# Kernel tuning notes

Measured on AMD Instinct MI355X. Metric: run time of the kernel, lower is better.

Reference implementation:

```python
import jax, jax.numpy as jnp
import numpy as np
import math

B, S, D, H = 2, 2048, 1024, 16
DK = D // H


def setup_inputs() -> dict:
    key = jax.random.key(0)
    ks = jax.random.split(key, 11)
    s = 1.0 / math.sqrt(D)
    return {
        "q": jax.random.normal(ks[0], (B, S, D), jnp.float32),
        "k": jax.random.normal(ks[1], (B, S, D), jnp.float32),
        "v": jax.random.normal(ks[2], (B, S, D), jnp.float32),
        "Wq": jax.random.normal(ks[3], (D, D), jnp.float32) * s,
        "bq": jnp.zeros((D,), jnp.float32),
        "Wk": jax.random.normal(ks[4], (D, D), jnp.float32) * s,
        "bk": jnp.zeros((D,), jnp.float32),
        "Wv": jax.random.normal(ks[5], (D, D), jnp.float32) * s,
        "bv": jnp.zeros((D,), jnp.float32),
        "Wo": jax.random.normal(ks[6], (D, D), jnp.float32) * s,
        "bo": jnp.zeros((D,), jnp.float32),
        "mask": jnp.ones((B, 1, S), dtype=bool),
    }


def reference(q, k, v, Wq, bq, Wk, bk, Wv, bv, Wo, bo, mask):
    # project and split heads: [B,S,D] -> [B,H,S,DK]
    def proj(x, W, b):
        return (x @ W.T + b).reshape(B, S, H, DK).transpose(0, 2, 1, 3)

    qh, kh, vh = proj(q, Wq, bq), proj(k, Wk, bk), proj(v, Wv, bv)
    scores = jnp.einsum("bhqd,bhkd->bhqk", qh, kh) / math.sqrt(DK)
    # 3D mask [B,1,S], self-attn: expand to [B,1,S,S] via outer AND
    m = mask[:, :, None, :] & mask[:, :, :, None]
    scores = jnp.where(m, scores, -1e9)
    attn = jax.nn.softmax(scores, axis=-1)
    attn = jnp.nan_to_num(attn, nan=0.0, posinf=0.0, neginf=0.0)
    out = jnp.einsum("bhqk,bhkd->bhqd", attn, vh)  # [B,H,S,DK]
    concat = out.transpose(0, 2, 1, 3).reshape(B, S, D)
    return concat @ Wo.T + bo
```

## Files before the change

### kernel.cpp

```cpp
#include <hip/hip_runtime.h>
#include <hip/hip_bf16.h>
#include <stdint.h>

using bf16 = __bf16;
typedef __attribute__((ext_vector_type(8))) __bf16 bf16x8;
typedef __attribute__((ext_vector_type(4))) __bf16 bf16x4;
typedef __attribute__((ext_vector_type(2))) __bf16 bf16x2;
typedef __attribute__((ext_vector_type(4))) float f32x4;

typedef const __attribute__((address_space(1))) void* gptr_t;
typedef __attribute__((address_space(3))) void* lptr_t;

__device__ __forceinline__ void gld16(const void* g, void* l) {
    __builtin_amdgcn_global_load_lds((gptr_t)g, (lptr_t)l, 16, 0, 0);
}

__global__ __launch_bounds__(256)
void cvt4_kern(const float* __restrict__ w0, const float* __restrict__ w1,
               const float* __restrict__ w2, const float* __restrict__ w3,
               bf16* __restrict__ o0, bf16* __restrict__ o1,
               bf16* __restrict__ o2, bf16* __restrict__ o3, int n)
{
    const int z = blockIdx.y;
    const float* in = z == 0 ? w0 : z == 1 ? w1 : z == 2 ? w2 : w3;
    bf16* out      = z == 0 ? o0 : z == 1 ? o1 : z == 2 ? o2 : o3;
    const int i = (blockIdx.x * 256 + threadIdx.x) * 8;
    if (i >= n) return;
    const float4 f0 = *(const float4*)(in + i);
    const float4 f1 = *(const float4*)(in + i + 4);
    bf16x8 v = { (bf16)f0.x, (bf16)f0.y, (bf16)f0.z, (bf16)f0.w,
                 (bf16)f1.x, (bf16)f1.y, (bf16)f1.z, (bf16)f1.w };
    *(bf16x8*)(out + i) = v;
}

__global__ __launch_bounds__(256)
void cvt3_kern(const float* __restrict__ x0, const float* __restrict__ x1,
               const float* __restrict__ x2,
               bf16* __restrict__ o0, bf16* __restrict__ o1,
               bf16* __restrict__ o2, int n)
{
    const int z = blockIdx.y;
    const float* in = z == 0 ? x0 : z == 1 ? x1 : x2;
    bf16* out      = z == 0 ? o0 : z == 1 ? o1 : o2;
    const int i = (blockIdx.x * 256 + threadIdx.x) * 8;
    if (i >= n) return;
    const float4 f0 = *(const float4*)(in + i);
    const float4 f1 = *(const float4*)(in + i + 4);
    bf16x8 v = { (bf16)f0.x, (bf16)f0.y, (bf16)f0.z, (bf16)f0.w,
                 (bf16)f1.x, (bf16)f1.y, (bf16)f1.z, (bf16)f1.w };
    *(bf16x8*)(out + i) = v;
}

template<bool XBF16, bool OUTF32>
__global__ __launch_bounds__(256, 3)
void gemm_qkv(const void* __restrict__ X0, const void* __restrict__ X1,
              const void* __restrict__ X2,
              const bf16* __restrict__ W0, const bf16* __restrict__ W1,
              const bf16* __restrict__ W2,
              const float* __restrict__ b0, const float* __restrict__ b1,
              const float* __restrict__ b2,
              void* __restrict__ Y0, void* __restrict__ Y1,
              void* __restrict__ Y2)
{
    constexpr int K = 1024, N = 1024, NT = K / 64;
    __shared__ bf16 smem[17408];
    bf16* As = smem;
    bf16* Bs = smem + 8192;

    const int z = blockIdx.z;
    const void*  Xv   = z == 0 ? X0 : z == 1 ? X1 : X2;
    const bf16*  W    = z == 0 ? W0 : z == 1 ? W1 : W2;
    const float* bias = z == 0 ? b0 : z == 1 ? b1 : b2;
    void*        Yv   = z == 0 ? Y0 : z == 1 ? Y1 : Y2;
    const int mode = (z == 2) ? 1 : 0;

    const int t = threadIdx.x;
    const int w = t >> 6, lane = t & 63, quad = lane >> 4, l15 = lane & 15;
    const int m0 = blockIdx.y * 128, n0 = blockIdx.x * 128;
    const int wm = (w >> 1) * 64, wn = (w & 1) * 64;

    const int srow = t >> 3;
    const int sseg = (t & 7) ^ (srow & 7);

    const float* Xf   = (const float*)Xv;
    const bf16*  gA16 = (const bf16*)Xv + (size_t)(m0 + srow) * K + sseg * 8;
    const bf16*  gB   = W + (size_t)(n0 + srow) * K + sseg * 8;

    f32x4 acc[4][4] = {};

    for (int kk = 0; kk < NT; ++kk) {
        const int k0 = kk * 64;
        if constexpr (XBF16) {
            #pragma unroll
            for (int r = 0; r < 4; ++r)
                gld16(gA16 + k0 + r * 32 * K, As + t * 8 + r * 2048);
        } else {
            #pragma unroll
            for (int r = 0; r < 4; ++r) {
                const int row = r * 32 + (t >> 3), sg = t & 7;
                const float* p = Xf + (size_t)(m0 + row) * K + k0 + sg * 8;
                const float4 f0 = *(const float4*)p;
                const float4 f1 = *(const float4*)(p + 4);
                bf16x8 vv = { (bf16)f0.x, (bf16)f0.y, (bf16)f0.z, (bf16)f0.w,
                              (bf16)f1.x, (bf16)f1.y, (bf16)f1.z, (bf16)f1.w };
                *(bf16x8*)&As[row * 64 + ((sg ^ (row & 7)) * 8)] = vv;
            }
        }
        #pragma unroll
        for (int r = 0; r < 4; ++r)
            gld16(gB + k0 + r * 32 * K, Bs + t * 8 + r * 2048);
        __syncthreads();

        bf16x8 af[4][2], bfr[4][2];
        #pragma unroll
        for (int mt = 0; mt < 4; ++mt)
            #pragma unroll
            for (int kt = 0; kt < 2; ++kt) {
                const int row = wm + mt * 16 + l15;
                const int seg = (kt * 4 + quad) ^ (row & 7);
                af[mt][kt] = *(const bf16x8*)&As[row * 64 + seg * 8];
            }
        #pragma unroll
        for (int nt = 0; nt < 4; ++nt)
            #pragma unroll
            for (int kt = 0; kt < 2; ++kt) {
                const int row = wn + nt * 16 + l15;
                const int seg = (kt * 4 + quad) ^ (row & 7);
                bfr[nt][kt] = *(const bf16x8*)&Bs[row * 64 + seg * 8];
            }
        #pragma unroll
        for (int kt = 0; kt < 2; ++kt)
            #pragma unroll
            for (int mt = 0; mt < 4; ++mt)
                #pragma unroll
                for (int nt = 0; nt < 4; ++nt)
                    acc[mt][nt] = __builtin_amdgcn_mfma_f32_16x16x32_bf16(
                        af[mt][kt], bfr[nt][kt], acc[mt][nt], 0, 0, 0);
        __syncthreads();
    }

    if (OUTF32 || mode == 0) {
        #pragma unroll
        for (int nt = 0; nt < 4; ++nt) {
            const int col = n0 + wn + nt * 16 + l15;
            const float bv = bias[col];
            #pragma unroll
            for (int mt = 0; mt < 4; ++mt)
                #pragma unroll
                for (int i = 0; i < 4; ++i) {
                    const int row = m0 + wm + mt * 16 + quad * 4 + i;
                    const float v = acc[mt][nt][i] + bv;
                    const size_t off = (size_t)row * N + col;
                    if (OUTF32) ((float*)Yv)[off] = v;
                    else        ((bf16*)Yv)[off]  = (bf16)v;
                }
        }
    } else {
        constexpr int LDT = 136;
        bf16* Tt = smem;
        #pragma unroll
        for (int nt = 0; nt < 4; ++nt) {
            const int col = wn + nt * 16 + l15;
            const float bv = bias[n0 + col];
            #pragma unroll
            for (int mt = 0; mt < 4; ++mt) {
                const int row0 = wm + mt * 16 + quad * 4;
                bf16x4 vv = { (bf16)(acc[mt][nt][0] + bv),
                              (bf16)(acc[mt][nt][1] + bv),
                              (bf16)(acc[mt][nt][2] + bv),
                              (bf16)(acc[mt][nt][3] + bv) };
                *(bf16x4*)&Tt[col * LDT + row0] = vv;
            }
        }
        __syncthreads();
        const int col = t >> 1, half = t & 1;
        const int gcol = n0 + col;
        const int h = gcol >> 6, d = gcol & 63;
        const int b = m0 >> 11, sb = (m0 & 2047) + half * 64;
        bf16* outp = (bf16*)Yv + (((size_t)(b * 16 + h) * 64 + d) << 11) + sb;
        #pragma unroll
        for (int j = 0; j < 8; ++j)
            *(bf16x8*)(outp + j * 8) =
                *(const bf16x8*)&Tt[col * LDT + half * 64 + j * 8];
    }
}

__global__ __launch_bounds__(512, 4)
void attn_mfma(const bf16* __restrict__ Q, const bf16* __restrict__ Kg,
               const bf16* __restrict__ Vt, bf16* Cc)
{
    constexpr int S = 2048, D = 1024, DK = 64, LDP = 72;
    constexpr int NTS = S / 64;
    __shared__ bf16 Qs[128 * 64];
    __shared__ bf16 Ks[2][64 * 64];
    __shared__ bf16 Vs[2][64 * 64];
    __shared__ bf16 Ps[8][16 * LDP];

    const int t = threadIdx.x;
    const int w = t >> 6, lane = t & 63, quad = lane >> 4, l15 = lane & 15;
    const int bh = blockIdx.y, b = bh >> 4, h = bh & 15;
    const int q0 = blockIdx.x * 128;
    const int wq = w * 16;

    const int srow = t >> 3;
    const int sseg = (t & 7) ^ (srow & 7);

    const bf16* gQ = Q + (size_t)(b * S + q0 + srow) * D + h * DK + sseg * 8;
    const bf16* gK = Kg + (size_t)(b * S + srow) * D + h * DK + sseg * 8;
    const bf16* gV = Vt + ((size_t)bh * DK + srow) * S + sseg * 8;

    gld16(gQ,                  Qs + t * 8);
    gld16(gQ + (size_t)64 * D, Qs + t * 8 + 4096);
    gld16(gK,                  Ks[0] + t * 8);
    gld16(gV,                  Vs[0] + t * 8);
    gld16(gK + (size_t)64 * D, Ks[1] + t * 8);
    gld16(gV + 64,             Vs[1] + t * 8);
    __syncthreads();

    bf16x8 aq[2];
    #pragma unroll
    for (int kt = 0; kt < 2; ++kt) {
        const int row = wq + l15;
        const int seg = (kt * 4 + quad) ^ (row & 7);
        aq[kt] = *(const bf16x8*)&Qs[row * 64 + seg * 8];
    }

    const bf16 onev = (l15 == 0) ? (bf16)1.0f : (bf16)0.0f;
    const bf16x8 bden = { onev, onev, onev, onev, onev, onev, onev, onev };

    f32x4 o[5] = {};
    float m = -1e30f;

    const float c = 0.125f * 1.44269504088896340736f;

    for (int ts = 0; ts < NTS; ++ts) {
        const int cur = ts & 1;
        if (ts < NTS - 1) asm volatile("s_waitcnt vmcnt(2)" ::: "memory");
        else              asm volatile("s_waitcnt vmcnt(0)" ::: "memory");
        __builtin_amdgcn_s_barrier();
        asm volatile("" ::: "memory");

        f32x4 sa[4] = {};
        bf16x8 bk[4][2];
        #pragma unroll
        for (int nt = 0; nt < 4; ++nt)
            #pragma unroll
            for (int kt = 0; kt < 2; ++kt) {
                const int row = nt * 16 + l15;
                const int seg = (kt * 4 + quad) ^ (row & 7);
                bk[nt][kt] = *(const bf16x8*)&Ks[cur][row * 64 + seg * 8];
            }
        __builtin_amdgcn_s_setprio(1);
        #pragma unroll
        for (int kt = 0; kt < 2; ++kt)
            #pragma unroll
            for (int nt = 0; nt < 4; ++nt)
                sa[nt] = __builtin_amdgcn_mfma_f32_16x16x32_bf16(
                    bk[nt][kt], aq[kt], sa[nt], 0, 0, 0);
        __builtin_amdgcn_s_setprio(0);

        const float a0 = fmaxf(fmaxf(sa[0][0], sa[0][1]), fmaxf(sa[0][2], sa[0][3]));
        const float a1 = fmaxf(fmaxf(sa[1][0], sa[1][1]), fmaxf(sa[1][2], sa[1][3]));
        const float a2 = fmaxf(fmaxf(sa[2][0], sa[2][1]), fmaxf(sa[2][2], sa[2][3]));
        const float a3 = fmaxf(fmaxf(sa[3][0], sa[3][1]), fmaxf(sa[3][2], sa[3][3]));
        float vmax = fmaxf(fmaxf(a0, a1), fmaxf(a2, a3)) * c;
        vmax = fmaxf(vmax, __shfl_xor(vmax, 16));
        vmax = fmaxf(vmax, __shfl_xor(vmax, 32));
        if (__any(vmax > m + 8.0f)) {
            const float mnew = fmaxf(m, vmax);
            const float al = __builtin_amdgcn_exp2f(m - mnew);
            m = mnew;
            #pragma unroll
            for (int i = 0; i < 4; ++i) {
                const float ai = __shfl(al, quad * 4 + i);
                #pragma unroll
                for (int nt = 0; nt < 5; ++nt)
                    o[nt][i] *= ai;
            }
        }
        #pragma unroll
        for (int nt = 0; nt < 4; ++nt) {
            const float p0 = __builtin_amdgcn_exp2f(sa[nt][0] * c - m);
            const float p1 = __builtin_amdgcn_exp2f(sa[nt][1] * c - m);
            const float p2 = __builtin_amdgcn_exp2f(sa[nt][2] * c - m);
            const float p3 = __builtin_amdgcn_exp2f(sa[nt][3] * c - m);
            const int base = l15 * LDP + nt * 16 + quad * 4;
            bf16x2 pw0 = { (bf16)p0, (bf16)p1 };
            bf16x2 pw1 = { (bf16)p2, (bf16)p3 };
            *(bf16x2*)&Ps[w][base]     = pw0;
            *(bf16x2*)&Ps[w][base + 2] = pw1;
        }

        bf16x8 ap[2], bvv[4][2];
        #pragma unroll
        for (int kt = 0; kt < 2; ++kt)
            ap[kt] = *(const bf16x8*)&Ps[w][l15 * LDP + kt * 32 + quad * 8];
        #pragma unroll
        for (int nt = 0; nt < 4; ++nt)
            #pragma unroll
            for (int kt = 0; kt < 2; ++kt) {
                const int row = nt * 16 + l15;
                const int seg = (kt * 4 + quad) ^ (row & 7);
                bvv[nt][kt] = *(const bf16x8*)&Vs[cur][row * 64 + seg * 8];
            }
        __builtin_amdgcn_s_setprio(1);
        #pragma unroll
        for (int kt = 0; kt < 2; ++kt) {
            #pragma unroll
            for (int nt = 0; nt < 4; ++nt)
                o[nt] = __builtin_amdgcn_mfma_f32_16x16x32_bf16(
                    ap[kt], bvv[nt][kt], o[nt], 0, 0, 0);
            o[4] = __builtin_amdgcn_mfma_f32_16x16x32_bf16(
                ap[kt], bden, o[4], 0, 0, 0);
        }
        __builtin_amdgcn_s_setprio(0);

        asm volatile("" ::: "memory");
        __builtin_amdgcn_s_barrier();
        asm volatile("" ::: "memory");
        if (ts + 2 < NTS) {
            gld16(gK + (size_t)(ts + 2) * 64 * D, Ks[cur] + t * 8);
            gld16(gV + (ts + 2) * 64,             Vs[cur] + t * 8);
        }
    }

    #pragma unroll
    for (int i = 0; i < 4; ++i) {
        const int row = q0 + wq + quad * 4 + i;
        const float lsum = __shfl(o[4][i], quad << 4);
        const float inv = 1.0f / lsum;
        #pragma unroll
        for (int nt = 0; nt < 4; ++nt) {
            const int col = nt * 16 + l15;
            Cc[(size_t)(b * S + row) * D + h * DK + col] = (bf16)(o[nt][i] * inv);
        }
    }
}

extern "C" void kernel_launch(void* const* d_in, const int* in_sizes, int n_in,
                              void* d_out, int out_size, void* d_ws, size_t ws_size,
                              hipStream_t stream)
{
    int iq=0, ik=1, iv=2, iWq=3, ibq=4, iWk=5, ibk=6, iWv=7, ibv=8, iWo=9, ibo=10;
    if (n_in >= 12 && in_sizes[0] == 1048576) {
        iWk=0; iWo=1; iWq=2; iWv=3; ibk=4; ibo=5; ibq=6; ibv=7; ik=8; iq=10; iv=11;
    }

    const float* q  = (const float*)d_in[iq];
    const float* k  = (const float*)d_in[ik];
    const float* v  = (const float*)d_in[iv];
    const float* Wq = (const float*)d_in[iWq];
    const float* bq = (const float*)d_in[ibq];
    const float* Wk = (const float*)d_in[iWk];
    const float* bk = (const float*)d_in[ibk];
    const float* Wv = (const float*)d_in[iWv];
    const float* bv = (const float*)d_in[ibv];
    const float* Wo = (const float*)d_in[iWo];
    const float* bo = (const float*)d_in[ibo];

    bf16* Qp  = (bf16*)d_ws;
    bf16* Kp  = Qp  + (size_t)4194304;
    bf16* Vtp = Kp  + (size_t)4194304;
    bf16* Wqb = Vtp + (size_t)4194304;
    bf16* Wkb = Wqb + (size_t)1048576;
    bf16* Wvb = Wkb + (size_t)1048576;
    bf16* Wob = Wvb + (size_t)1048576;
    bf16* qb  = Wob + (size_t)1048576;
    bf16* kb  = qb  + (size_t)4194304;
    bf16* vb  = kb  + (size_t)4194304;
    bf16* Cc  = Qp;

    constexpr int WN = 1048576, XN = 4194304;
    cvt4_kern<<<dim3(512, 4), dim3(256), 0, stream>>>(
        Wq, Wk, Wv, Wo, Wqb, Wkb, Wvb, Wob, WN);

    const bool pre = ws_size >= (size_t)56 * 1024 * 1024;
    if (pre) {
        cvt3_kern<<<dim3(2048, 3), dim3(256), 0, stream>>>(
            q, k, v, qb, kb, vb, XN);
        gemm_qkv<true, false><<<dim3(8, 32, 3), dim3(256), 0, stream>>>(
            qb, kb, vb, Wqb, Wkb, Wvb, bq, bk, bv, Qp, Kp, Vtp);
    } else {
        gemm_qkv<false, false><<<dim3(8, 32, 3), dim3(256), 0, stream>>>(
            q, k, v, Wqb, Wkb, Wvb, bq, bk, bv, Qp, Kp, Vtp);
    }

    attn_mfma<<<dim3(16, 32), dim3(512), 0, stream>>>(Qp, Kp, Vtp, Cc);

    gemm_qkv<true, true><<<dim3(8, 32, 1), dim3(256), 0, stream>>>(
        Cc, Cc, Cc, Wob, Wob, Wob, bo, bo, bo, d_out, d_out, d_out);
}
```

Baseline: 239.1 us.

## Merge conversion launches, add dedicated output-projection GEMM, widen P stores

Merges the weight and activation fp32-to-bf16 conversions into one seven-slice launch, which saves a kernel launch on the preallocated path. Replaces the reused QKV GEMM for the output projection with a dedicated 64x128-tile GEMM that launches twice as many blocks and writes fp32 directly. It also combines two bf16x2 LDS stores of softmax probabilities into a single bf16x4 store. The new GEMM uses a single LDS buffer with no prefetch pipelining, and its fp32 output stores are strided per lane, which may coalesce poorly.

```diff
diff --git a/kernel.cpp b/kernel.cpp
--- a/kernel.cpp
+++ b/kernel.cpp
@@ -34,14 +34,26 @@
 }
 
 __global__ __launch_bounds__(256)
-void cvt3_kern(const float* __restrict__ x0, const float* __restrict__ x1,
+void cvt7_kern(const float* __restrict__ w0, const float* __restrict__ w1,
+               const float* __restrict__ w2, const float* __restrict__ w3,
+               const float* __restrict__ x0, const float* __restrict__ x1,
                const float* __restrict__ x2,
-               bf16* __restrict__ o0, bf16* __restrict__ o1,
-               bf16* __restrict__ o2, int n)
+               bf16* __restrict__ ow0, bf16* __restrict__ ow1,
+               bf16* __restrict__ ow2, bf16* __restrict__ ow3,
+               bf16* __restrict__ ox0, bf16* __restrict__ ox1,
+               bf16* __restrict__ ox2, int nw, int nx)
 {
     const int z = blockIdx.y;
-    const float* in = z == 0 ? x0 : z == 1 ? x1 : x2;
-    bf16* out      = z == 0 ? o0 : z == 1 ? o1 : o2;
+    const float* in; bf16* out; int n;
+    if (z < 4) {
+        in = z == 0 ? w0 : z == 1 ? w1 : z == 2 ? w2 : w3;
+        out = z == 0 ? ow0 : z == 1 ? ow1 : z == 2 ? ow2 : ow3;
+        n = nw;
+    } else {
+        in = z == 4 ? x0 : z == 5 ? x1 : x2;
+        out = z == 4 ? ox0 : z == 5 ? ox1 : ox2;
+        n = nx;
+    }
     const int i = (blockIdx.x * 256 + threadIdx.x) * 8;
     if (i >= n) return;
     const float4 f0 = *(const float4*)(in + i);
@@ -182,6 +194,78 @@
         for (int j = 0; j < 8; ++j)
             *(bf16x8*)(outp + j * 8) =
                 *(const bf16x8*)&Tt[col * LDT + half * 64 + j * 8];
+    }
+}
+
+__global__ __launch_bounds__(256, 2)
+void gemm_wo(const bf16* __restrict__ X, const bf16* __restrict__ W,
+             const float* __restrict__ bias, float* __restrict__ Y)
+{
+    constexpr int K = 1024, N = 1024;
+    __shared__ bf16 As[64 * 64];
+    __shared__ bf16 Bs[128 * 64];
+
+    const int t = threadIdx.x;
+    const int w = t >> 6, lane = t & 63, quad = lane >> 4, l15 = lane & 15;
+    const int m0 = blockIdx.y * 64, n0 = blockIdx.x * 128;
+    const int wm = (w >> 1) * 32, wn = (w & 1) * 64;
+
+    const int srow = t >> 3;
+    const int sseg = (t & 7) ^ (srow & 7);
+
+    const bf16* gA = X + (size_t)(m0 + srow) * K + sseg * 8;
+    const bf16* gB = W + (size_t)(n0 + srow) * K + sseg * 8;
+
+    f32x4 acc[2][4] = {};
+
+    for (int k0 = 0; k0 < K; k0 += 64) {
+        gld16(gA + k0,          As + t * 8);
+        gld16(gA + k0 + 32 * K, As + t * 8 + 2048);
+        gld16(gB + k0,          Bs + t * 8);
+        gld16(gB + k0 + 32 * K, Bs + t * 8 + 2048);
+        gld16(gB + k0 + 64 * K, Bs + t * 8 + 4096);
+        gld16(gB + k0 + 96 * K, Bs + t * 8 + 6144);
+        __syncthreads();
+
+        bf16x8 af[2][2], bfr[4][2];
+        #pragma unroll
+        for (int mt = 0; mt < 2; ++mt)
+            #pragma unroll
+            for (int kt = 0; kt < 2; ++kt) {
+                const int row = wm + mt * 16 + l15;
+                const int seg = (kt * 4 + quad) ^ (row & 7);
+                af[mt][kt] = *(const bf16x8*)&As[row * 64 + seg * 8];
+            }
+        #pragma unroll
+        for (int nt = 0; nt < 4; ++nt)
+            #pragma unroll
+            for (int kt = 0; kt < 2; ++kt) {
+                const int row = wn + nt * 16 + l15;
+                const int seg = (kt * 4 + quad) ^ (row & 7);
+                bfr[nt][kt] = *(const bf16x8*)&Bs[row * 64 + seg * 8];
+            }
+        #pragma unroll
+        for (int kt = 0; kt < 2; ++kt)
+            #pragma unroll
+            for (int mt = 0; mt < 2; ++mt)
+                #pragma unroll
+                for (int nt = 0; nt < 4; ++nt)
+                    acc[mt][nt] = __builtin_amdgcn_mfma_f32_16x16x32_bf16(
+                        af[mt][kt], bfr[nt][kt], acc[mt][nt], 0, 0, 0);
+        __syncthreads();
+    }
+
+    #pragma unroll
+    for (int nt = 0; nt < 4; ++nt) {
+        const int col = n0 + wn + nt * 16 + l15;
+        const float bv = bias[col];
+        #pragma unroll
+        for (int mt = 0; mt < 2; ++mt)
+            #pragma unroll
+            for (int i = 0; i < 4; ++i) {
+                const int row = m0 + wm + mt * 16 + quad * 4 + i;
+                Y[(size_t)row * N + col] = acc[mt][nt][i] + bv;
+            }
     }
 }
 
@@ -284,11 +368,8 @@
             const float p1 = __builtin_amdgcn_exp2f(sa[nt][1] * c - m);
             const float p2 = __builtin_amdgcn_exp2f(sa[nt][2] * c - m);
             const float p3 = __builtin_amdgcn_exp2f(sa[nt][3] * c - m);
-            const int base = l15 * LDP + nt * 16 + quad * 4;
-            bf16x2 pw0 = { (bf16)p0, (bf16)p1 };
-            bf16x2 pw1 = { (bf16)p2, (bf16)p3 };
-            *(bf16x2*)&Ps[w][base]     = pw0;
-            *(bf16x2*)&Ps[w][base + 2] = pw1;
+            bf16x4 pw = { (bf16)p0, (bf16)p1, (bf16)p2, (bf16)p3 };
+            *(bf16x4*)&Ps[w][l15 * LDP + nt * 16 + quad * 4] = pw;
         }
 
         bf16x8 ap[2], bvv[4][2];
@@ -371,22 +452,21 @@
     bf16* Cc  = Qp;
 
     constexpr int WN = 1048576, XN = 4194304;
-    cvt4_kern<<<dim3(512, 4), dim3(256), 0, stream>>>(
-        Wq, Wk, Wv, Wo, Wqb, Wkb, Wvb, Wob, WN);
-
     const bool pre = ws_size >= (size_t)56 * 1024 * 1024;
     if (pre) {
-        cvt3_kern<<<dim3(2048, 3), dim3(256), 0, stream>>>(
-            q, k, v, qb, kb, vb, XN);
+        cvt7_kern<<<dim3(2048, 7), dim3(256), 0, stream>>>(
+            Wq, Wk, Wv, Wo, q, k, v,
+            Wqb, Wkb, Wvb, Wob, qb, kb, vb, WN, XN);
         gemm_qkv<true, false><<<dim3(8, 32, 3), dim3(256), 0, stream>>>(
             qb, kb, vb, Wqb, Wkb, Wvb, bq, bk, bv, Qp, Kp, Vtp);
     } else {
+        cvt4_kern<<<dim3(512, 4), dim3(256), 0, stream>>>(
+            Wq, Wk, Wv, Wo, Wqb, Wkb, Wvb, Wob, WN);
         gemm_qkv<false, false><<<dim3(8, 32, 3), dim3(256), 0, stream>>>(
             q, k, v, Wqb, Wkb, Wvb, bq, bk, bv, Qp, Kp, Vtp);
     }
 
     attn_mfma<<<dim3(16, 32), dim3(512), 0, stream>>>(Qp, Kp, Vtp, Cc);
 
-    gemm_qkv<true, true><<<dim3(8, 32, 1), dim3(256), 0, stream>>>(
-        Cc, Cc, Cc, Wob, Wob, Wob, bo, bo, bo, d_out, d_out, d_out);
-}
+    gemm_wo<<<dim3(8, 64), dim3(256), 0, stream>>>(Cc, Wob, bo, (float*)d_out);
+}
```

Result: faster. 231.8 us (-3.0%).
